# Optimization experiments

Hardware: AMD Instinct MI355X
Metric: run time of the kernel (lower is better)

## Reference

```python
import jax, jax.numpy as jnp
import numpy as np
import math

D_MODEL = 1024
NUM_HEADS = 16
D_K = 64
B, T = 2, 2048


def setup_inputs() -> dict:
    key = jax.random.key(0)
    ks = jax.random.split(key, 12)
    s = 0.02
    return {
        "Q": jax.random.normal(ks[0], (B, T, D_MODEL), jnp.float32),
        "K": jax.random.normal(ks[1], (B, T, D_MODEL), jnp.float32),
        "V": jax.random.normal(ks[2], (B, T, D_MODEL), jnp.float32),
        # stacked per-head projection weights: [H, d_model, d_k]
        "Wq": jax.random.normal(ks[3], (NUM_HEADS, D_MODEL, D_K), jnp.float32) * s,
        "bq": jax.random.normal(ks[4], (NUM_HEADS, D_K), jnp.float32) * s,
        "Wk": jax.random.normal(ks[5], (NUM_HEADS, D_MODEL, D_K), jnp.float32) * s,
        "bk": jax.random.normal(ks[6], (NUM_HEADS, D_K), jnp.float32) * s,
        "Wv": jax.random.normal(ks[7], (NUM_HEADS, D_MODEL, D_K), jnp.float32) * s,
        "bv": jax.random.normal(ks[8], (NUM_HEADS, D_K), jnp.float32) * s,
        "Wo": jax.random.normal(ks[9], (D_MODEL, D_MODEL), jnp.float32) * s,
        "bo": jax.random.normal(ks[10], (D_MODEL,), jnp.float32) * s,
    }


def reference(Q, K, V, Wq, bq, Wk, bk, Wv, bv, Wo, bo):
    scale = 1.0 / math.sqrt(D_K)
    # fused batched per-head projections (replaces the Python per-head loop)
    Qh = jnp.einsum("btd,hdk->bhtk", Q, Wq) + bq[None, :, None, :]
    Kh = jnp.einsum("btd,hdk->bhtk", K, Wk) + bk[None, :, None, :]
    Vh = jnp.einsum("btd,hdk->bhtk", V, Wv) + bv[None, :, None, :]
    scores = jnp.einsum("bhtk,bhsk->bhts", Qh, Kh) * scale  # [B,H,T,T]
    attn = jax.nn.softmax(scores, axis=-1)
    ctx = jnp.einsum("bhts,bhsk->bhtk", attn, Vh)  # [B,H,T,d_k]
    # Faithful to the original: plain view of contiguous [B,H,T,d] into
    # [B,T,H*d] WITHOUT transposing head/time (matches torch .view semantics).
    bsz, nt = Q.shape[0], Q.shape[1]
    x = ctx.reshape(bsz, nt, NUM_HEADS * D_K)
    out = x @ Wo.T + bo
    # dropout with p=0.0 is identity; omitted for determinism
    return out
```

## Files before the change

kernel.cpp:

```cpp
#include <hip/hip_runtime.h>
#include <stdint.h>

typedef __attribute__((ext_vector_type(8))) short short8;
typedef __attribute__((ext_vector_type(4))) short short4v;
typedef __attribute__((ext_vector_type(4))) float float4v;

#define MFMA16(a, b, c) __builtin_amdgcn_mfma_f32_16x16x32_bf16((a), (b), (c), 0, 0, 0)

__device__ __forceinline__ ushort f2bf_rne(float f) {
  union { float f; unsigned u; } x; x.f = f;
  unsigned r = x.u + 0x7FFFu + ((x.u >> 16) & 1u);
  return (ushort)(r >> 16);
}
__device__ __forceinline__ ushort f2bf_trunc(float f) {
  union { float f; unsigned u; } x; x.f = f;
  return (ushort)(x.u >> 16);
}
__device__ __forceinline__ void gload16(const ushort* g, ushort* lds) {
  __builtin_amdgcn_global_load_lds(
      (__attribute__((address_space(1))) unsigned int*)g,
      (__attribute__((address_space(3))) unsigned int*)lds, 16, 0, 0);
}

#define CEXP 0.1803368801111204f

__device__ __forceinline__ void transpose64f(const float* __restrict__ in, int is,
                                             ushort* __restrict__ out, int os,
                                             ushort* lds ) {
  const int t = threadIdx.x;
#pragma unroll
  for (int it = 0; it < 2; ++it) {
    int e = it * 2048 + t * 8;
    int r = e >> 6, c = e & 63;
    const float* p = in + (size_t)r * is + c;
    float4 x0 = *(const float4*)p;
    float4 x1 = *(const float4*)(p + 4);
    ushort tv[8] __attribute__((aligned(16))) = {
        f2bf_rne(x0.x), f2bf_rne(x0.y), f2bf_rne(x0.z), f2bf_rne(x0.w),
        f2bf_rne(x1.x), f2bf_rne(x1.y), f2bf_rne(x1.z), f2bf_rne(x1.w)};
    *(uint4*)&lds[r * 72 + c] = *(const uint4*)tv;
  }
  __syncthreads();
  const int cc = t >> 2;
  const int rg = (t & 3) * 16;
  ushort tmp[16] __attribute__((aligned(16)));
#pragma unroll
  for (int i = 0; i < 16; ++i) tmp[i] = lds[(rg + i) * 72 + cc];
  *(uint4*)&out[(size_t)cc * os + rg] = *(const uint4*)&tmp[0];
  *(uint4*)&out[(size_t)cc * os + rg + 8] = *(const uint4*)&tmp[8];
}

__global__ __launch_bounds__(256) void prep_kernel(
    const float* __restrict__ Q, const float* __restrict__ K,
    const float* __restrict__ V, const float* __restrict__ Wo,
    const float* __restrict__ Wq, const float* __restrict__ Wk,
    const float* __restrict__ Wv, ushort* __restrict__ Qb, ushort* __restrict__ Kb,
    ushort* __restrict__ Vb, ushort* __restrict__ WoB, ushort* __restrict__ BtQ,
    ushort* __restrict__ BtK, ushort* __restrict__ BtV) {
  __shared__ ushort lds[64 * 72];
  const int bx = blockIdx.x;
  if (bx < 6656) {
    const float* s;
    ushort* d;
    int i;
    if (bx < 6144) {
      const int plane = bx >> 11;
      s = plane == 0 ? Q : (plane == 1 ? K : V);
      d = plane == 0 ? Qb : (plane == 1 ? Kb : Vb);
      i = ((bx & 2047) * 256 + threadIdx.x) * 8;
    } else {
      s = Wo;
      d = WoB;
      i = ((bx - 6144) * 256 + threadIdx.x) * 8;
    }
    float4 a = *(const float4*)(s + i);
    float4 b = *(const float4*)(s + i + 4);
    ushort t[8] __attribute__((aligned(16))) = {
        f2bf_rne(a.x), f2bf_rne(a.y), f2bf_rne(a.z), f2bf_rne(a.w),
        f2bf_rne(b.x), f2bf_rne(b.y), f2bf_rne(b.z), f2bf_rne(b.w)};
    *(uint4*)(d + i) = *(const uint4*)t;
  } else {
    const int rb = bx - 6656;
    const int dt = rb & 15, h = (rb >> 4) & 15, z = rb >> 8;
    const float* W = z == 0 ? Wq : (z == 1 ? Wk : Wv);
    ushort* Bt = z == 0 ? BtQ : (z == 1 ? BtK : BtV);
    transpose64f(W + h * 65536 + dt * 4096, 64, Bt + h * 65536 + dt * 64, 1024, lds);
  }
}

__global__ __launch_bounds__(256, 2) void repack_w_kernel(
    const float* __restrict__ Wq, const float* __restrict__ Wk,
    const float* __restrict__ Wv, ushort* __restrict__ BtQ, ushort* __restrict__ BtK,
    ushort* __restrict__ BtV) {
  __shared__ ushort lds[64 * 72];
  const float* W = blockIdx.z == 0 ? Wq : (blockIdx.z == 1 ? Wk : Wv);
  ushort* Bt = blockIdx.z == 0 ? BtQ : (blockIdx.z == 1 ? BtK : BtV);
  const int h = blockIdx.y, dt = blockIdx.x;
  transpose64f(W + h * 65536 + dt * 4096, 64, Bt + h * 65536 + dt * 64, 1024, lds);
}

__device__ __forceinline__ void gemm_pipe(const ushort* __restrict__ A,
                                          const ushort* __restrict__ Bt,
                                          const float* __restrict__ bias,
                                          void* __restrict__ C, int cmode, float ascale,
                                          int N, int K, ushort* lA, ushort* lB) {
  const int tid = threadIdx.x;
  const int l = tid & 63, lane15 = l & 15, quad = l >> 4;
  const int mbase = blockIdx.y * 128, nbase = blockIdx.x * 128;
  const int wv = tid >> 6;
  const int wrow = (wv >> 1) * 64, wcol = (wv & 1) * 64;

  const int e0 = tid * 8;
  const int e1 = 2048 + tid * 8;
  const int r0 = e0 >> 5, c0 = e0 & 31;
  const int r1 = e1 >> 5, c1 = e1 & 31;
  const ushort* Ag0 = A + (size_t)(mbase + r0) * K + c0;
  const ushort* Ag1 = A + (size_t)(mbase + r1) * K + c1;
  const ushort* Bg0 = Bt + (size_t)(nbase + r0) * K + c0;
  const ushort* Bg1 = Bt + (size_t)(nbase + r1) * K + c1;

  float4v acc[4][4];
#pragma unroll
  for (int i = 0; i < 4; ++i)
#pragma unroll
    for (int j = 0; j < 4; ++j) acc[i][j] = (float4v){0.f, 0.f, 0.f, 0.f};

  gload16(Ag0, lA + e0);
  gload16(Ag1, lA + e1);
  gload16(Bg0, lB + e0);
  gload16(Bg1, lB + e1);

  for (int kb = 0; kb < K; kb += 32) {
    const int p = (kb >> 5) & 1;
    const int kn = (kb + 32 < K) ? kb + 32 : 0;
    const int q = (p ^ 1) * 4096;
    gload16(Ag0 + kn, lA + q + e0);
    gload16(Ag1 + kn, lA + q + e1);
    gload16(Bg0 + kn, lB + q + e0);
    gload16(Bg1 + kn, lB + q + e1);
    asm volatile("s_waitcnt vmcnt(4)\ns_barrier" ::: "memory");
    const int base = p * 4096;
    short8 a[4], b[4];
#pragma unroll
    for (int i = 0; i < 4; ++i) {
      a[i] = *(const short8*)&lA[base + (wrow + i * 16 + lane15) * 32 + quad * 8];
      b[i] = *(const short8*)&lB[base + (wcol + i * 16 + lane15) * 32 + quad * 8];
    }
#pragma unroll
    for (int i = 0; i < 4; ++i)
#pragma unroll
      for (int j = 0; j < 4; ++j) acc[i][j] = MFMA16(a[i], b[j], acc[i][j]);
    asm volatile("s_waitcnt lgkmcnt(0)\ns_barrier" ::: "memory");
  }

  if (cmode == 1) {
    asm volatile("s_waitcnt vmcnt(0) lgkmcnt(0)\ns_barrier" ::: "memory");
    uint* sp = (uint*)lA + wv * 576;
    const int bb = mbase >> 11;
    const int tb = (mbase & 2047) + wrow;
#pragma unroll
    for (int j = 0; j < 4; ++j) {
      {
        const int n = nbase + wcol + j * 16 + lane15;
        const float bvs = bias[n];
#pragma unroll
        for (int i = 0; i < 4; ++i)
#pragma unroll
          for (int rp = 0; rp < 2; ++rp) {
            const uint lo = f2bf_rne((acc[i][j][2 * rp] + bvs) * ascale);
            const uint hi = f2bf_rne((acc[i][j][2 * rp + 1] + bvs) * ascale);
            sp[36 * lane15 + i * 8 + quad * 2 + rp] = lo | (hi << 16);
          }
      }
#pragma unroll
      for (int t = 0; t < 2; ++t) {
        const int row = t * 8 + (l >> 3);
        const int c = l & 7;
        uint4 d = *(const uint4*)(sp + 36 * row + 4 * c);
        const int ng = nbase + wcol + j * 16 + row;
        ushort* dst = (ushort*)C + ((size_t)(bb * 1024 + ng)) * 2048 + tb + c * 8;
        *(uint4*)dst = d;
      }
    }
    return;
  }

#pragma unroll
  for (int j = 0; j < 4; ++j) {
    const int n = nbase + wcol + j * 16 + lane15;
    const float bvs = bias[n];
#pragma unroll
    for (int i = 0; i < 4; ++i) {
      const int m0 = mbase + wrow + i * 16 + quad * 4;
#pragma unroll
      for (int r = 0; r < 4; ++r) {
        const float val = (acc[i][j][r] + bvs) * ascale;
        if (cmode == 2)
          ((float*)C)[(size_t)(m0 + r) * N + n] = val;
        else
          ((ushort*)C)[(size_t)(m0 + r) * N + n] = f2bf_rne(val);
      }
    }
  }
}

__global__ __launch_bounds__(256, 2) void proj3_kernel(
    const ushort* __restrict__ Qb, const ushort* __restrict__ Kb,
    const ushort* __restrict__ Vb, const ushort* __restrict__ BtQ,
    const ushort* __restrict__ BtK, const ushort* __restrict__ BtV,
    const float* __restrict__ bq, const float* __restrict__ bk,
    const float* __restrict__ bv, ushort* __restrict__ Qh, ushort* __restrict__ Kh,
    ushort* __restrict__ Vt) {
  __shared__ ushort lA[2 * 4096], lB[2 * 4096];
  const ushort *Aop, *Bop;
  const float* bs;
  ushort* Cp;
  int cm;
  float as;
  if (blockIdx.z == 0) { Aop = Qb; Bop = BtQ; bs = bq; Cp = Qh; cm = 0; as = CEXP; }
  else if (blockIdx.z == 1) { Aop = Kb; Bop = BtK; bs = bk; Cp = Kh; cm = 0; as = 1.0f; }
  else { Aop = Vb; Bop = BtV; bs = bv; Cp = Vt; cm = 1; as = 1.0f; }
  gemm_pipe(Aop, Bop, bs, Cp, cm, as, 1024, 1024, lA, lB);
}

__global__ __launch_bounds__(256, 2) void gemm_bt_kernel(
    const ushort* __restrict__ X, const ushort* __restrict__ WoB,
    const float* __restrict__ bo, float* __restrict__ out) {
  __shared__ ushort lA[2 * 4096], lB[2 * 4096];
  gemm_pipe(X, WoB, bo, out, 2, 1.0f, 1024, 1024, lA, lB);
}

template <int F32>
__device__ __forceinline__ void stage16(const void* G, size_t eoff, ushort* ldst) {
  if (F32) {
    const float* p = (const float*)G + eoff;
    float4 x0 = *(const float4*)p;
    float4 x1 = *(const float4*)(p + 4);
    ushort t[8] __attribute__((aligned(16))) = {
        f2bf_rne(x0.x), f2bf_rne(x0.y), f2bf_rne(x0.z), f2bf_rne(x0.w),
        f2bf_rne(x1.x), f2bf_rne(x1.y), f2bf_rne(x1.z), f2bf_rne(x1.w)};
    *(uint4*)ldst = *(const uint4*)t;
  } else {
    gload16((const ushort*)G + eoff, ldst);
  }
}

template <int AF32, int BF32>
__device__ __forceinline__ void gemm_body_basic(const void* __restrict__ A,
                                                const void* __restrict__ Bt,
                                                const float* __restrict__ bias,
                                                void* __restrict__ C, int cmode,
                                                float ascale, int N, int K, ushort* lA,
                                                ushort* lB) {
  const int tid = threadIdx.x;
  const int l = tid & 63, lane15 = l & 15, quad = l >> 4;
  const int mbase = blockIdx.y * 128, nbase = blockIdx.x * 128;
  const int w = tid >> 6;
  const int wrow = (w >> 1) * 64, wcol = (w & 1) * 64;
  const int e0 = tid * 8;
  const int e1 = 2048 + tid * 8;
  const int r0 = e0 >> 5, c0 = e0 & 31;
  const int r1 = e1 >> 5, c1 = e1 & 31;

  float4v acc[4][4];
#pragma unroll
  for (int i = 0; i < 4; ++i)
#pragma unroll
    for (int j = 0; j < 4; ++j) acc[i][j] = (float4v){0.f, 0.f, 0.f, 0.f};

  for (int kb = 0; kb < K; kb += 32) {
    __syncthreads();
    stage16<AF32>(A, (size_t)(mbase + r0) * K + c0 + kb, &lA[e0]);
    stage16<AF32>(A, (size_t)(mbase + r1) * K + c1 + kb, &lA[e1]);
    stage16<BF32>(Bt, (size_t)(nbase + r0) * K + c0 + kb, &lB[e0]);
    stage16<BF32>(Bt, (size_t)(nbase + r1) * K + c1 + kb, &lB[e1]);
    asm volatile("s_waitcnt vmcnt(0)" ::: "memory");
    __syncthreads();
    short8 a[4], b[4];
#pragma unroll
    for (int i = 0; i < 4; ++i) {
      a[i] = *(const short8*)&lA[(wrow + i * 16 + lane15) * 32 + quad * 8];
      b[i] = *(const short8*)&lB[(wcol + i * 16 + lane15) * 32 + quad * 8];
    }
#pragma unroll
    for (int i = 0; i < 4; ++i)
#pragma unroll
      for (int j = 0; j < 4; ++j) acc[i][j] = MFMA16(a[i], b[j], acc[i][j]);
  }

#pragma unroll
  for (int j = 0; j < 4; ++j) {
    const int n = nbase + wcol + j * 16 + lane15;
    const float bvs = bias[n];
#pragma unroll
    for (int i = 0; i < 4; ++i) {
      const int m0 = mbase + wrow + i * 16 + quad * 4;
#pragma unroll
      for (int r = 0; r < 4; ++r) {
        const float val = (acc[i][j][r] + bvs) * ascale;
        if (cmode == 1) {
          const int m = m0 + r;
          const int bb = m >> 11, t = m & 2047;
          ((ushort*)C)[((size_t)(bb * 1024 + n)) * 2048 + t] = f2bf_rne(val);
        } else if (cmode == 2) {
          ((float*)C)[(size_t)(m0 + r) * N + n] = val;
        } else {
          ((ushort*)C)[(size_t)(m0 + r) * N + n] = f2bf_rne(val);
        }
      }
    }
  }
}

__global__ __launch_bounds__(256, 2) void proj3f_kernel(
    const float* __restrict__ Q, const float* __restrict__ Kin,
    const float* __restrict__ V, const ushort* __restrict__ BtQ,
    const ushort* __restrict__ BtK, const ushort* __restrict__ BtV,
    const float* __restrict__ bq, const float* __restrict__ bk,
    const float* __restrict__ bv, ushort* __restrict__ Qh, ushort* __restrict__ Kh,
    ushort* __restrict__ Vt) {
  __shared__ ushort lA[128 * 32], lB[128 * 32];
  if (blockIdx.z == 0)
    gemm_body_basic<1, 0>(Q, BtQ, bq, Qh, 0, CEXP, 1024, 1024, lA, lB);
  else if (blockIdx.z == 1)
    gemm_body_basic<1, 0>(Kin, BtK, bk, Kh, 0, 1.0f, 1024, 1024, lA, lB);
  else
    gemm_body_basic<1, 0>(V, BtV, bv, Vt, 1, 1.0f, 1024, 1024, lA, lB);
}

__global__ __launch_bounds__(256, 2) void gemm_btf_kernel(
    const ushort* __restrict__ X, const float* __restrict__ Wo,
    const float* __restrict__ bo, float* __restrict__ out) {
  __shared__ ushort lA[128 * 32], lB[128 * 32];
  gemm_body_basic<0, 1>(X, Wo, bo, out, 2, 1.0f, 1024, 1024, lA, lB);
}

__global__ __launch_bounds__(256, 3) void attn_kernel(const ushort* __restrict__ Qh,
                                                      const ushort* __restrict__ Kh,
                                                      const ushort* __restrict__ Vt,
                                                      ushort* __restrict__ ctxout) {
  __shared__ ushort lK[2 * 4096];
  __shared__ ushort lV[2 * 4096];
  __shared__ ushort pl_all[4][16 * 68];
  const int tid = threadIdx.x, l = tid & 63, wv = tid >> 6;
  const int lane15 = l & 15, quad = l >> 4;
  const int bh = blockIdx.x, b = bh >> 4, h = bh & 15;
  const int q0 = blockIdx.y * 64 + wv * 16;

  const int sr = tid >> 3;
  const int scb = (tid & 7) ^ (sr & 7);
  const ushort* Kp = Kh + (size_t)(b * 2048) * 1024 + h * 64;
  const ushort* Vp = Vt + (size_t)(bh * 64) * 2048;
  const ushort* Kg0 = Kp + (size_t)sr * 1024 + scb * 8;
  const ushort* Kg1 = Kg0 + 32 * 1024;
  const ushort* Vg0 = Vp + (size_t)sr * 2048 + scb * 8;
  const ushort* Vg1 = Vg0 + 32 * 2048;

  const ushort* qrow = Qh + (size_t)(b * 2048 + q0 + lane15) * 1024 + h * 64;
  const short8 qa0 = *(const short8*)&qrow[quad * 8];
  const short8 qa1 = *(const short8*)&qrow[32 + quad * 8];

  const int xm = lane15 & 7;
  const int fr0 = lane15 * 64 + ((quad ^ xm) * 8);
  const int fr1 = lane15 * 64 + (((quad + 4) ^ xm) * 8);

  ushort* pl = &pl_all[wv][0];
  const short8 ones = {0x3F80, 0x3F80, 0x3F80, 0x3F80, 0x3F80, 0x3F80, 0x3F80, 0x3F80};

  float4v o[4];
  float4v lf = (float4v){0.f, 0.f, 0.f, 0.f};
#pragma unroll
  for (int i = 0; i < 4; ++i) o[i] = (float4v){0.f, 0.f, 0.f, 0.f};

  gload16(Kg0, lK + tid * 8);
  gload16(Kg1, lK + 2048 + tid * 8);
  gload16(Vg0, lV + tid * 8);
  gload16(Vg1, lV + 2048 + tid * 8);

  for (int s0 = 0; s0 < 2048; s0 += 64) {
    const int p = (s0 >> 6) & 1;
    const int sn = (s0 + 64 < 2048) ? s0 + 64 : 0;
    const int q = (p ^ 1) * 4096;
    gload16(Kg0 + (size_t)sn * 1024, lK + q + tid * 8);
    gload16(Kg1 + (size_t)sn * 1024, lK + q + 2048 + tid * 8);
    gload16(Vg0 + sn, lV + q + tid * 8);
    gload16(Vg1 + sn, lV + q + 2048 + tid * 8);
    asm volatile("s_waitcnt vmcnt(4)\ns_barrier" ::: "memory");
    const int base = p * 4096;

    float4v sb[4];
#pragma unroll
    for (int i = 0; i < 4; ++i) {
      short8 k0 = *(const short8*)&lK[base + i * 1024 + fr0];
      short8 k1 = *(const short8*)&lK[base + i * 1024 + fr1];
      float4v c = (float4v){0.f, 0.f, 0.f, 0.f};
      c = MFMA16(qa0, k0, c);
      c = MFMA16(qa1, k1, c);
      sb[i] = c;
    }
#pragma unroll
    for (int i = 0; i < 4; ++i)
#pragma unroll
      for (int r = 0; r < 4; ++r)
        pl[(quad * 4 + r) * 68 + i * 16 + lane15] =
            f2bf_trunc(__builtin_amdgcn_exp2f(sb[i][r]));
    short4v p0a = *(const short4v*)&pl[lane15 * 68 + quad * 8];
    short4v p0b = *(const short4v*)&pl[lane15 * 68 + quad * 8 + 4];
    short4v p1a = *(const short4v*)&pl[lane15 * 68 + 32 + quad * 8];
    short4v p1b = *(const short4v*)&pl[lane15 * 68 + 32 + quad * 8 + 4];
    short8 pa0 = __builtin_shufflevector(p0a, p0b, 0, 1, 2, 3, 4, 5, 6, 7);
    short8 pa1 = __builtin_shufflevector(p1a, p1b, 0, 1, 2, 3, 4, 5, 6, 7);
    lf = MFMA16(pa0, ones, lf);
    lf = MFMA16(pa1, ones, lf);
#pragma unroll
    for (int nf = 0; nf < 4; ++nf) {
      short8 v0 = *(const short8*)&lV[base + nf * 1024 + fr0];
      short8 v1 = *(const short8*)&lV[base + nf * 1024 + fr1];
      o[nf] = MFMA16(pa0, v0, o[nf]);
      o[nf] = MFMA16(pa1, v1, o[nf]);
    }
    asm volatile("s_waitcnt lgkmcnt(0)\ns_barrier" ::: "memory");
  }

  float inv[4];
#pragma unroll
  for (int r = 0; r < 4; ++r) inv[r] = (lf[r] > 0.f) ? 1.0f / lf[r] : 0.0f;
  ushort* crow = ctxout + ((size_t)bh * 2048 + q0) * 64;
#pragma unroll
  for (int nf = 0; nf < 4; ++nf)
#pragma unroll
    for (int r = 0; r < 4; ++r)
      crow[(size_t)(quad * 4 + r) * 64 + nf * 16 + lane15] = f2bf_rne(o[nf][r] * inv[r]);
}

extern "C" void kernel_launch(void* const* d_in, const int* in_sizes, int n_in,
                              void* d_out, int out_size, void* d_ws, size_t ws_size,
                              hipStream_t stream) {
  const float* Q = (const float*)d_in[0];
  const float* K = (const float*)d_in[1];
  const float* V = (const float*)d_in[2];
  const float* Wq = (const float*)d_in[3];
  const float* bq = (const float*)d_in[4];
  const float* Wk = (const float*)d_in[5];
  const float* bk = (const float*)d_in[6];
  const float* Wv = (const float*)d_in[7];
  const float* bv = (const float*)d_in[8];
  const float* Wo = (const float*)d_in[9];
  const float* bo = (const float*)d_in[10];
  float* out = (float*)d_out;
  ushort* ws = (ushort*)d_ws;

  if (ws_size >= (58ull << 20)) {
    ushort* Qh = ws;
    ushort* Kh = Qh + (4 << 20);
    ushort* Vt = Kh + (4 << 20);
    ushort* BtQ = Vt + (4 << 20);
    ushort* BtK = BtQ + (1 << 20);
    ushort* BtV = BtK + (1 << 20);
    ushort* X = BtQ;
    ushort* WoB = ws + (16ull << 20);
    ushort* Qb = WoB + (1 << 20);
    ushort* Kb = Qb + (4 << 20);
    ushort* Vb = Kb + (4 << 20);

    prep_kernel<<<dim3(7424), 256, 0, stream>>>(Q, K, V, Wo, Wq, Wk, Wv, Qb, Kb, Vb,
                                                WoB, BtQ, BtK, BtV);
    proj3_kernel<<<dim3(8, 32, 3), 256, 0, stream>>>(Qb, Kb, Vb, BtQ, BtK, BtV, bq, bk,
                                                     bv, Qh, Kh, Vt);
    attn_kernel<<<dim3(32, 32), 256, 0, stream>>>(Qh, Kh, Vt, X);
    gemm_bt_kernel<<<dim3(8, 32), 256, 0, stream>>>(X, WoB, bo, out);
  } else {
    ushort* Qh = ws;
    ushort* Kh = Qh + (4 << 20);
    ushort* Vt = Kh + (4 << 20);
    ushort* R = Vt + (4 << 20);
    ushort* BtQ = R;
    ushort* BtK = R + (1 << 20);
    ushort* BtV = R + (2 << 20);
    ushort* X = R;

    repack_w_kernel<<<dim3(16, 16, 3), 256, 0, stream>>>(Wq, Wk, Wv, BtQ, BtK, BtV);
    proj3f_kernel<<<dim3(8, 32, 3), 256, 0, stream>>>(Q, K, V, BtQ, BtK, BtV, bq, bk, bv,
                                                      Qh, Kh, Vt);
    attn_kernel<<<dim3(32, 32), 256, 0, stream>>>(Qh, Kh, Vt, X);
    gemm_btf_kernel<<<dim3(8, 32), 256, 0, stream>>>(X, Wo, bo, out);
  }
}
```

Before: 243.6 us.

## Drop double-buffered pipelines for single-buffer loops, retile output GEMM, raise attention occupancy

Removes the double-buffered gemm_pipe path and reroutes the projections through the single-buffered gemm_body_basic, which gains a new transposed-V epilogue mode. The output projection becomes a dedicated kernel with 128x64 tiles and twice as many blocks. Attention now stages K/V into a single buffer with a full wait each step and asks for four blocks per SM instead of three. The intent is to trade load/compute overlap for lower LDS use and higher occupancy, at the risk of exposing global-load latency on every iteration.

```diff
diff --git a/kernel.cpp b/kernel.cpp
--- a/kernel.cpp
+++ b/kernel.cpp
@@ -99,137 +99,6 @@
   transpose64f(W + h * 65536 + dt * 4096, 64, Bt + h * 65536 + dt * 64, 1024, lds);
 }
 
-__device__ __forceinline__ void gemm_pipe(const ushort* __restrict__ A,
-                                          const ushort* __restrict__ Bt,
-                                          const float* __restrict__ bias,
-                                          void* __restrict__ C, int cmode, float ascale,
-                                          int N, int K, ushort* lA, ushort* lB) {
-  const int tid = threadIdx.x;
-  const int l = tid & 63, lane15 = l & 15, quad = l >> 4;
-  const int mbase = blockIdx.y * 128, nbase = blockIdx.x * 128;
-  const int wv = tid >> 6;
-  const int wrow = (wv >> 1) * 64, wcol = (wv & 1) * 64;
-
-  const int e0 = tid * 8;
-  const int e1 = 2048 + tid * 8;
-  const int r0 = e0 >> 5, c0 = e0 & 31;
-  const int r1 = e1 >> 5, c1 = e1 & 31;
-  const ushort* Ag0 = A + (size_t)(mbase + r0) * K + c0;
-  const ushort* Ag1 = A + (size_t)(mbase + r1) * K + c1;
-  const ushort* Bg0 = Bt + (size_t)(nbase + r0) * K + c0;
-  const ushort* Bg1 = Bt + (size_t)(nbase + r1) * K + c1;
-
-  float4v acc[4][4];
-#pragma unroll
-  for (int i = 0; i < 4; ++i)
-#pragma unroll
-    for (int j = 0; j < 4; ++j) acc[i][j] = (float4v){0.f, 0.f, 0.f, 0.f};
-
-  gload16(Ag0, lA + e0);
-  gload16(Ag1, lA + e1);
-  gload16(Bg0, lB + e0);
-  gload16(Bg1, lB + e1);
-
-  for (int kb = 0; kb < K; kb += 32) {
-    const int p = (kb >> 5) & 1;
-    const int kn = (kb + 32 < K) ? kb + 32 : 0;
-    const int q = (p ^ 1) * 4096;
-    gload16(Ag0 + kn, lA + q + e0);
-    gload16(Ag1 + kn, lA + q + e1);
-    gload16(Bg0 + kn, lB + q + e0);
-    gload16(Bg1 + kn, lB + q + e1);
-    asm volatile("s_waitcnt vmcnt(4)\ns_barrier" ::: "memory");
-    const int base = p * 4096;
-    short8 a[4], b[4];
-#pragma unroll
-    for (int i = 0; i < 4; ++i) {
-      a[i] = *(const short8*)&lA[base + (wrow + i * 16 + lane15) * 32 + quad * 8];
-      b[i] = *(const short8*)&lB[base + (wcol + i * 16 + lane15) * 32 + quad * 8];
-    }
-#pragma unroll
-    for (int i = 0; i < 4; ++i)
-#pragma unroll
-      for (int j = 0; j < 4; ++j) acc[i][j] = MFMA16(a[i], b[j], acc[i][j]);
-    asm volatile("s_waitcnt lgkmcnt(0)\ns_barrier" ::: "memory");
-  }
-
-  if (cmode == 1) {
-    asm volatile("s_waitcnt vmcnt(0) lgkmcnt(0)\ns_barrier" ::: "memory");
-    uint* sp = (uint*)lA + wv * 576;
-    const int bb = mbase >> 11;
-    const int tb = (mbase & 2047) + wrow;
-#pragma unroll
-    for (int j = 0; j < 4; ++j) {
-      {
-        const int n = nbase + wcol + j * 16 + lane15;
-        const float bvs = bias[n];
-#pragma unroll
-        for (int i = 0; i < 4; ++i)
-#pragma unroll
-          for (int rp = 0; rp < 2; ++rp) {
-            const uint lo = f2bf_rne((acc[i][j][2 * rp] + bvs) * ascale);
-            const uint hi = f2bf_rne((acc[i][j][2 * rp + 1] + bvs) * ascale);
-            sp[36 * lane15 + i * 8 + quad * 2 + rp] = lo | (hi << 16);
-          }
-      }
-#pragma unroll
-      for (int t = 0; t < 2; ++t) {
-        const int row = t * 8 + (l >> 3);
-        const int c = l & 7;
-        uint4 d = *(const uint4*)(sp + 36 * row + 4 * c);
-        const int ng = nbase + wcol + j * 16 + row;
-        ushort* dst = (ushort*)C + ((size_t)(bb * 1024 + ng)) * 2048 + tb + c * 8;
-        *(uint4*)dst = d;
-      }
-    }
-    return;
-  }
-
-#pragma unroll
-  for (int j = 0; j < 4; ++j) {
-    const int n = nbase + wcol + j * 16 + lane15;
-    const float bvs = bias[n];
-#pragma unroll
-    for (int i = 0; i < 4; ++i) {
-      const int m0 = mbase + wrow + i * 16 + quad * 4;
-#pragma unroll
-      for (int r = 0; r < 4; ++r) {
-        const float val = (acc[i][j][r] + bvs) * ascale;
-        if (cmode == 2)
-          ((float*)C)[(size_t)(m0 + r) * N + n] = val;
-        else
-          ((ushort*)C)[(size_t)(m0 + r) * N + n] = f2bf_rne(val);
-      }
-    }
-  }
-}
-
-__global__ __launch_bounds__(256, 2) void proj3_kernel(
-    const ushort* __restrict__ Qb, const ushort* __restrict__ Kb,
-    const ushort* __restrict__ Vb, const ushort* __restrict__ BtQ,
-    const ushort* __restrict__ BtK, const ushort* __restrict__ BtV,
-    const float* __restrict__ bq, const float* __restrict__ bk,
-    const float* __restrict__ bv, ushort* __restrict__ Qh, ushort* __restrict__ Kh,
-    ushort* __restrict__ Vt) {
-  __shared__ ushort lA[2 * 4096], lB[2 * 4096];
-  const ushort *Aop, *Bop;
-  const float* bs;
-  ushort* Cp;
-  int cm;
-  float as;
-  if (blockIdx.z == 0) { Aop = Qb; Bop = BtQ; bs = bq; Cp = Qh; cm = 0; as = CEXP; }
-  else if (blockIdx.z == 1) { Aop = Kb; Bop = BtK; bs = bk; Cp = Kh; cm = 0; as = 1.0f; }
-  else { Aop = Vb; Bop = BtV; bs = bv; Cp = Vt; cm = 1; as = 1.0f; }
-  gemm_pipe(Aop, Bop, bs, Cp, cm, as, 1024, 1024, lA, lB);
-}
-
-__global__ __launch_bounds__(256, 2) void gemm_bt_kernel(
-    const ushort* __restrict__ X, const ushort* __restrict__ WoB,
-    const float* __restrict__ bo, float* __restrict__ out) {
-  __shared__ ushort lA[2 * 4096], lB[2 * 4096];
-  gemm_pipe(X, WoB, bo, out, 2, 1.0f, 1024, 1024, lA, lB);
-}
-
 template <int F32>
 __device__ __forceinline__ void stage16(const void* G, size_t eoff, ushort* ldst) {
   if (F32) {
@@ -288,6 +157,38 @@
       for (int j = 0; j < 4; ++j) acc[i][j] = MFMA16(a[i], b[j], acc[i][j]);
   }
 
+  if (cmode == 3) {
+    __syncthreads();
+    uint* sp = (uint*)lA + w * 576;
+    const int bb = mbase >> 11;
+    const int tb = (mbase & 2047) + wrow;
+#pragma unroll
+    for (int j = 0; j < 4; ++j) {
+      {
+        const int n = nbase + wcol + j * 16 + lane15;
+        const float bvs = bias[n];
+#pragma unroll
+        for (int i = 0; i < 4; ++i)
+#pragma unroll
+          for (int rp = 0; rp < 2; ++rp) {
+            const uint lo = f2bf_rne((acc[i][j][2 * rp] + bvs) * ascale);
+            const uint hi = f2bf_rne((acc[i][j][2 * rp + 1] + bvs) * ascale);
+            sp[36 * lane15 + i * 8 + quad * 2 + rp] = lo | (hi << 16);
+          }
+      }
+#pragma unroll
+      for (int t = 0; t < 2; ++t) {
+        const int row = t * 8 + (l >> 3);
+        const int c = l & 7;
+        uint4 d = *(const uint4*)(sp + 36 * row + 4 * c);
+        const int ng = nbase + wcol + j * 16 + row;
+        ushort* dst = (ushort*)C + ((size_t)(bb * 1024 + ng)) * 2048 + tb + c * 8;
+        *(uint4*)dst = d;
+      }
+    }
+    return;
+  }
+
 #pragma unroll
   for (int j = 0; j < 4; ++j) {
     const int n = nbase + wcol + j * 16 + lane15;
@@ -312,6 +213,78 @@
   }
 }
 
+__global__ __launch_bounds__(256, 2) void proj3_kernel(
+    const ushort* __restrict__ Qb, const ushort* __restrict__ Kb,
+    const ushort* __restrict__ Vb, const ushort* __restrict__ BtQ,
+    const ushort* __restrict__ BtK, const ushort* __restrict__ BtV,
+    const float* __restrict__ bq, const float* __restrict__ bk,
+    const float* __restrict__ bv, ushort* __restrict__ Qh, ushort* __restrict__ Kh,
+    ushort* __restrict__ Vt) {
+  __shared__ ushort lA[5120], lB[4096];
+  if (blockIdx.z == 0)
+    gemm_body_basic<0, 0>(Qb, BtQ, bq, Qh, 0, CEXP, 1024, 1024, lA, lB);
+  else if (blockIdx.z == 1)
+    gemm_body_basic<0, 0>(Kb, BtK, bk, Kh, 0, 1.0f, 1024, 1024, lA, lB);
+  else
+    gemm_body_basic<0, 0>(Vb, BtV, bv, Vt, 3, 1.0f, 1024, 1024, lA, lB);
+}
+
+__global__ __launch_bounds__(256, 2) void gemm_out_kernel(
+    const ushort* __restrict__ X, const ushort* __restrict__ WoB,
+    const float* __restrict__ bo, float* __restrict__ out) {
+  __shared__ ushort lA[4096], lB[2048];
+  const int tid = threadIdx.x;
+  const int l = tid & 63, lane15 = l & 15, quad = l >> 4;
+  const int mbase = blockIdx.y * 128, nbase = blockIdx.x * 64;
+  const int wv = tid >> 6;
+  const int wrow = wv * 32;
+  const int e0 = tid * 8;
+  const int e1 = 2048 + tid * 8;
+  const int r0 = e0 >> 5, c0 = e0 & 31;
+  const int r1 = e1 >> 5, c1 = e1 & 31;
+  const ushort* Ag0 = X + (size_t)(mbase + r0) * 1024 + c0;
+  const ushort* Ag1 = X + (size_t)(mbase + r1) * 1024 + c1;
+  const ushort* Bg0 = WoB + (size_t)(nbase + r0) * 1024 + c0;
+
+  float4v acc[2][4];
+#pragma unroll
+  for (int i = 0; i < 2; ++i)
+#pragma unroll
+    for (int j = 0; j < 4; ++j) acc[i][j] = (float4v){0.f, 0.f, 0.f, 0.f};
+
+  for (int kb = 0; kb < 1024; kb += 32) {
+    __syncthreads();
+    gload16(Ag0 + kb, &lA[e0]);
+    gload16(Ag1 + kb, &lA[e1]);
+    gload16(Bg0 + kb, &lB[e0]);
+    asm volatile("s_waitcnt vmcnt(0)" ::: "memory");
+    __syncthreads();
+    short8 a[2], b[4];
+#pragma unroll
+    for (int i = 0; i < 2; ++i)
+      a[i] = *(const short8*)&lA[(wrow + i * 16 + lane15) * 32 + quad * 8];
+#pragma unroll
+    for (int j = 0; j < 4; ++j)
+      b[j] = *(const short8*)&lB[(j * 16 + lane15) * 32 + quad * 8];
+#pragma unroll
+    for (int i = 0; i < 2; ++i)
+#pragma unroll
+      for (int j = 0; j < 4; ++j) acc[i][j] = MFMA16(a[i], b[j], acc[i][j]);
+  }
+
+#pragma unroll
+  for (int j = 0; j < 4; ++j) {
+    const int n = nbase + j * 16 + lane15;
+    const float bvs = bo[n];
+#pragma unroll
+    for (int i = 0; i < 2; ++i) {
+      const int m0 = mbase + wrow + i * 16 + quad * 4;
+#pragma unroll
+      for (int r = 0; r < 4; ++r) out[(size_t)(m0 + r) * 1024 + n] = acc[i][j][r] + bvs;
+    }
+  }
+}
+
 __global__ __launch_bounds__(256, 2) void proj3f_kernel(
     const float* __restrict__ Q, const float* __restrict__ Kin,
     const float* __restrict__ V, const ushort* __restrict__ BtQ,
@@ -319,28 +292,28 @@
     const float* __restrict__ bq, const float* __restrict__ bk,
     const float* __restrict__ bv, ushort* __restrict__ Qh, ushort* __restrict__ Kh,
     ushort* __restrict__ Vt) {
-  __shared__ ushort lA[128 * 32], lB[128 * 32];
+  __shared__ ushort lA[5120], lB[4096];
   if (blockIdx.z == 0)
     gemm_body_basic<1, 0>(Q, BtQ, bq, Qh, 0, CEXP, 1024, 1024, lA, lB);
   else if (blockIdx.z == 1)
     gemm_body_basic<1, 0>(Kin, BtK, bk, Kh, 0, 1.0f, 1024, 1024, lA, lB);
   else
-    gemm_body_basic<1, 0>(V, BtV, bv, Vt, 1, 1.0f, 1024, 1024, lA, lB);
+    gemm_body_basic<1, 0>(V, BtV, bv, Vt, 3, 1.0f, 1024, 1024, lA, lB);
 }
 
 __global__ __launch_bounds__(256, 2) void gemm_btf_kernel(
     const ushort* __restrict__ X, const float* __restrict__ Wo,
     const float* __restrict__ bo, float* __restrict__ out) {
-  __shared__ ushort lA[128 * 32], lB[128 * 32];
+  __shared__ ushort lA[5120], lB[4096];
   gemm_body_basic<0, 1>(X, Wo, bo, out, 2, 1.0f, 1024, 1024, lA, lB);
 }
 
-__global__ __launch_bounds__(256, 3) void attn_kernel(const ushort* __restrict__ Qh,
+__global__ __launch_bounds__(256, 4) void attn_kernel(const ushort* __restrict__ Qh,
                                                       const ushort* __restrict__ Kh,
                                                       const ushort* __restrict__ Vt,
                                                       ushort* __restrict__ ctxout) {
-  __shared__ ushort lK[2 * 4096];
-  __shared__ ushort lV[2 * 4096];
+  __shared__ ushort lK[64 * 64];
+  __shared__ ushort lV[64 * 64];
   __shared__ ushort pl_all[4][16 * 68];
   const int tid = threadIdx.x, l = tid & 63, wv = tid >> 6;
   const int lane15 = l & 15, quad = l >> 4;
@@ -355,6 +328,10 @@
   const ushort* Kg1 = Kg0 + 32 * 1024;
   const ushort* Vg0 = Vp + (size_t)sr * 2048 + scb * 8;
   const ushort* Vg1 = Vg0 + 32 * 2048;
+  ushort* lKd0 = lK + tid * 8;
+  ushort* lKd1 = lK + 2048 + tid * 8;
+  ushort* lVd0 = lV + tid * 8;
+  ushort* lVd1 = lV + 2048 + tid * 8;
 
   const ushort* qrow = Qh + (size_t)(b * 2048 + q0 + lane15) * 1024 + h * 64;
   const short8 qa0 = *(const short8*)&qrow[quad * 8];
@@ -372,27 +349,20 @@
 #pragma unroll
   for (int i = 0; i < 4; ++i) o[i] = (float4v){0.f, 0.f, 0.f, 0.f};
 
-  gload16(Kg0, lK + tid * 8);
-  gload16(Kg1, lK + 2048 + tid * 8);
-  gload16(Vg0, lV + tid * 8);
-  gload16(Vg1, lV + 2048 + tid * 8);
-
   for (int s0 = 0; s0 < 2048; s0 += 64) {
-    const int p = (s0 >> 6) & 1;
-    const int sn = (s0 + 64 < 2048) ? s0 + 64 : 0;
-    const int q = (p ^ 1) * 4096;
-    gload16(Kg0 + (size_t)sn * 1024, lK + q + tid * 8);
-    gload16(Kg1 + (size_t)sn * 1024, lK + q + 2048 + tid * 8);
-    gload16(Vg0 + sn, lV + q + tid * 8);
-    gload16(Vg1 + sn, lV + q + 2048 + tid * 8);
-    asm volatile("s_waitcnt vmcnt(4)\ns_barrier" ::: "memory");
-    const int base = p * 4096;
+    __syncthreads();
+    gload16(Kg0 + (size_t)s0 * 1024, lKd0);
+    gload16(Kg1 + (size_t)s0 * 1024, lKd1);
+    gload16(Vg0 + s0, lVd0);
+    gload16(Vg1 + s0, lVd1);
+    asm volatile("s_waitcnt vmcnt(0)" ::: "memory");
+    __syncthreads();
 
     float4v sb[4];
 #pragma unroll
     for (int i = 0; i < 4; ++i) {
-      short8 k0 = *(const short8*)&lK[base + i * 1024 + fr0];
-      short8 k1 = *(const short8*)&lK[base + i * 1024 + fr1];
+      short8 k0 = *(const short8*)&lK[i * 1024 + fr0];
+      short8 k1 = *(const short8*)&lK[i * 1024 + fr1];
       float4v c = (float4v){0.f, 0.f, 0.f, 0.f};
       c = MFMA16(qa0, k0, c);
       c = MFMA16(qa1, k1, c);
@@ -414,12 +384,11 @@
     lf = MFMA16(pa1, ones, lf);
 #pragma unroll
     for (int nf = 0; nf < 4; ++nf) {
-      short8 v0 = *(const short8*)&lV[base + nf * 1024 + fr0];
-      short8 v1 = *(const short8*)&lV[base + nf * 1024 + fr1];
+      short8 v0 = *(const short8*)&lV[nf * 1024 + fr0];
+      short8 v1 = *(const short8*)&lV[nf * 1024 + fr1];
       o[nf] = MFMA16(pa0, v0, o[nf]);
       o[nf] = MFMA16(pa1, v1, o[nf]);
     }
-    asm volatile("s_waitcnt lgkmcnt(0)\ns_barrier" ::: "memory");
   }
 
   float inv[4];
@@ -468,7 +437,7 @@
     proj3_kernel<<<dim3(8, 32, 3), 256, 0, stream>>>(Qb, Kb, Vb, BtQ, BtK, BtV, bq, bk,
                                                      bv, Qh, Kh, Vt);
     attn_kernel<<<dim3(32, 32), 256, 0, stream>>>(Qh, Kh, Vt, X);
-    gemm_bt_kernel<<<dim3(8, 32), 256, 0, stream>>>(X, WoB, bo, out);
+    gemm_out_kernel<<<dim3(16, 32), 256, 0, stream>>>(X, WoB, bo, out);
   } else {
     ushort* Qh = ws;
     ushort* Kh = Qh + (4 << 20);
```

Result: faster. 228.8 us (-6.1%).
